# Optimization experiments

Hardware: AMD Instinct MI355X
Metric: run time of the kernel (lower is better)

Reference implementation:

```python
import jax, jax.numpy as jnp
import numpy as np

RAD_ORDER = 15
ANG_ORDER = 7
RAD_CUTOFF = 6.0
ANG_CUTOFF = 4.0
MIN_CUTOFF = 0.55
N_SPECIES = 2
N_ATOMS = 10000
MAX_NB = 32


def _typespin(n_species):
    # matches Fortran: even n skips zero -> {-1, 1} for 2 species
    vals = []
    s = int(-n_species / 2)
    for _ in range(n_species):
        if s == 0 and n_species % 2 == 0:
            s += 1
        vals.append(float(s))
        s += 1
    return jnp.asarray(vals, dtype=jnp.float32)


def _cheby_stack(x, order):
    # T_0..T_order of x, stacked on last axis
    Ts = [jnp.ones_like(x), x]
    for _ in range(2, order + 1):
        Ts.append(2.0 * x * Ts[-1] - Ts[-2])
    return jnp.stack(Ts[: order + 1], axis=-1)


def setup_inputs() -> dict:
    key = jax.random.key(0)
    k1, k2, k3 = jax.random.split(key, 3)
    positions = jax.random.normal(k1, (N_ATOMS, 3), dtype=jnp.float32) * 5.0
    species_indices = jax.random.randint(k2, (N_ATOMS,), 0, N_SPECIES)
    neighbor_indices = jax.random.randint(k3, (N_ATOMS, MAX_NB), 0, N_ATOMS)
    neighbor_vectors = jax.random.normal(jax.random.fold_in(key, 7), (N_ATOMS, MAX_NB, 3), dtype=jnp.float32) * 2.5
    return {
        "positions": positions,
        "species_indices": species_indices,
        "neighbor_indices": neighbor_indices,
        "neighbor_vectors": neighbor_vectors,
    }


def _features(positions, species_indices, neighbor_indices, neighbor_vectors):
    typespin = _typespin(N_SPECIES)
    ts_nb = typespin[species_indices[neighbor_indices]]  # [N, M]

    d = jnp.linalg.norm(neighbor_vectors, axis=-1)  # [N, M]
    d_safe = jnp.maximum(d, 1e-8)

    # ---------- radial ----------
    mask_r = ((d <= RAD_CUTOFF) & (d > MIN_CUTOFF)).astype(d.dtype)  # [N, M]
    x_r = jnp.clip(2.0 * (d - MIN_CUTOFF) / (RAD_CUTOFF - MIN_CUTOFF) - 1.0, -1.0, 1.0)
    fc_r = 0.5 * (jnp.cos(jnp.pi * jnp.minimum(d, RAD_CUTOFF) / RAD_CUTOFF) + 1.0)
    G_rad = _cheby_stack(x_r, RAD_ORDER) * (fc_r * mask_r)[..., None]  # [N, M, n_rad]
    rad_unw = G_rad.sum(axis=1)                          # [N, n_rad]
    rad_w = (G_rad * ts_nb[..., None]).sum(axis=1)       # [N, n_rad]

    # ---------- angular ----------
    mask_a = ((d <= ANG_CUTOFF) & (d > MIN_CUTOFF)).astype(d.dtype)  # [N, M]
    fc_a = 0.5 * (jnp.cos(jnp.pi * jnp.minimum(d, ANG_CUTOFF) / ANG_CUTOFF) + 1.0) * mask_a
    unit = neighbor_vectors / d_safe[..., None]          # [N, M, 3]
    cos = jnp.clip(jnp.einsum("nmd,nkd->nmk", unit, unit), -1.0, 1.0)  # [N, M, M]
    triu = jnp.triu(jnp.ones((MAX_NB, MAX_NB), dtype=d.dtype), k=1)
    w = fc_a[:, :, None] * fc_a[:, None, :] * triu       # [N, M, M] pair weight, j<k only
    w_ts = w * ts_nb[:, :, None] * ts_nb[:, None, :]

    # Chebyshev recurrence over cos(theta); accumulate per order to avoid [N,M,M,n_ang]
    ang_unw, ang_w = [], []
    T_prev = jnp.ones_like(cos)
    T_cur = cos
    for n in range(ANG_ORDER + 1):
        T_n = T_prev if n == 0 else (T_cur if n == 1 else 2.0 * cos * T_cur - T_prev)
        if n >= 2:
            T_prev, T_cur = T_cur, T_n
        ang_unw.append(jnp.einsum("nmk,nmk->n", w, T_n))
        ang_w.append(jnp.einsum("nmk,nmk->n", w_ts, T_n))
    ang_unw = jnp.stack(ang_unw, axis=1)  # [N, n_ang]
    ang_w = jnp.stack(ang_w, axis=1)

    # feature layout: [rad_unweighted, rad_typespin, ang_unweighted, ang_typespin]
    return jnp.concatenate([rad_unw, rad_w, ang_unw, ang_w], axis=1)  # [N, 48]


def reference(positions, species_indices, neighbor_indices, neighbor_vectors):
    return _features(positions, species_indices, neighbor_indices, neighbor_vectors)
```

## Files before the change

kernel.cpp:

```cpp
#include <hip/hip_runtime.h>

#define NATOMS 10000
#define MAXNB  32
#define NRAD   16
#define NANG   8
#define WPB    4
#define RSTRIDE 33

__global__ __launch_bounds__(256, 4) void cheby_desc_kernel(
    const int*   __restrict__ species,
    const int*   __restrict__ nb_idx,
    const float* __restrict__ nb_vec,
    float*       __restrict__ out)
{
    const int lane = threadIdx.x & 63;
    const int wv   = threadIdx.x >> 6;
    const int atom = blockIdx.x * WPB + wv;
    const int nb   = lane & 31;

    __shared__ float nbd[WPB][MAXNB][5];
    __shared__ float red[WPB][64][RSTRIDE];

    const float vx = nb_vec[(atom * MAXNB + nb) * 3 + 0];
    const float vy = nb_vec[(atom * MAXNB + nb) * 3 + 1];
    const float vz = nb_vec[(atom * MAXNB + nb) * 3 + 2];
    const int   ni = nb_idx[atom * MAXNB + nb];
    const float ts = (float)(2 * species[ni] - 1);

    const float d     = __builtin_amdgcn_sqrtf(vx * vx + vy * vy + vz * vz);
    const float inv_d = __builtin_amdgcn_rcpf(fmaxf(d, 1e-8f));
    const float ux = vx * inv_d, uy = vy * inv_d, uz = vz * inv_d;

    const float PI = 3.14159265358979323846f;

    float xr = 2.0f * (d - 0.55f) * (1.0f / (6.0f - 0.55f)) - 1.0f;
    xr = fminf(fmaxf(xr, -1.0f), 1.0f);
    const float fcr = 0.5f * (__cosf(fminf(d, 6.0f) * (PI / 6.0f)) + 1.0f);
    float g = ((d <= 6.0f) && (d > 0.55f)) ? fcr : 0.0f;
    if (lane >= 32) g *= ts;

    float rad[NRAD];
    {
        rad[0] = g;
        rad[1] = g * xr;
        float Tp = 1.0f, Tc = xr;
        const float x2 = xr + xr;
        #pragma unroll
        for (int n = 2; n < NRAD; ++n) {
            const float Tn = x2 * Tc - Tp;
            rad[n] = g * Tn;
            Tp = Tc; Tc = Tn;
        }
    }

    const float fca = ((d <= 4.0f) && (d > 0.55f))
                    ? 0.5f * (__cosf(fminf(d, 4.0f) * (PI / 4.0f)) + 1.0f) : 0.0f;
    const float fcats = fca * ts;

    if (lane < 32) {
        nbd[wv][nb][0] = ux;  nbd[wv][nb][1] = uy;  nbd[wv][nb][2] = uz;
        nbd[wv][nb][3] = fca; nbd[wv][nb][4] = fcats;
    }
    __syncthreads();

    float aU[NANG], aW[NANG];
    #pragma unroll
    for (int n = 0; n < NANG; ++n) { aU[n] = 0.0f; aW[n] = 0.0f; }

    const int half = lane >> 5;
    #pragma unroll
    for (int it = 0; it < 8; ++it) {
        const int o = 2 * it + 1 + half;
        const int k = (nb + o) & 31;
        const float kx   = nbd[wv][k][0];
        const float ky   = nbd[wv][k][1];
        const float kz   = nbd[wv][k][2];
        const float fk   = nbd[wv][k][3];
        const float fkts = nbd[wv][k][4];
        float c = ux * kx + uy * ky + uz * kz;
        c = fminf(fmaxf(c, -1.0f), 1.0f);
        float w   = fca   * fk;
        float wts = fcats * fkts;
        if (o == 16) { w *= 0.5f; wts *= 0.5f; }
        const float c2 = c + c;
        float Ta = 1.0f, Tb = c;
        aU[0] += w;     aW[0] += wts;
        aU[1] += w * c; aW[1] += wts * c;
        #pragma unroll
        for (int n = 2; n < NANG; ++n) {
            const float Tn = c2 * Tb - Ta;
            aU[n] += w * Tn;  aW[n] += wts * Tn;
            Ta = Tb; Tb = Tn;
        }
    }

    {
        float* rrow = &red[wv][lane][0];
        #pragma unroll
        for (int n = 0; n < NRAD; ++n) rrow[n] = rad[n];
        #pragma unroll
        for (int n = 0; n < NANG; ++n) { rrow[16 + n] = aU[n]; rrow[24 + n] = aW[n]; }
    }
    __syncthreads();

    const int   base = ((lane >> 4) & 1) * 32;
    const int   col  = (lane < 32) ? (lane & 15) : (16 + (lane & 15));
    const float* rcol = &red[wv][base][col];
    float s0 = 0.0f, s1 = 0.0f, s2 = 0.0f, s3 = 0.0f;
    #pragma unroll
    for (int i = 0; i < 32; i += 4) {
        s0 += rcol[(i + 0) * RSTRIDE];
        s1 += rcol[(i + 1) * RSTRIDE];
        s2 += rcol[(i + 2) * RSTRIDE];
        s3 += rcol[(i + 3) * RSTRIDE];
    }
    float v = (s0 + s1) + (s2 + s3);
    const float vp = __shfl_xor(v, 16, 64);
    if (lane >= 32) v += vp;
    if (lane < 48) out[atom * 48 + lane] = v;
}

extern "C" void kernel_launch(void* const* d_in, const int* in_sizes, int n_in,
                              void* d_out, int out_size, void* d_ws, size_t ws_size,
                              hipStream_t stream) {
    const int*   species = (const int*)  d_in[1];
    const int*   nbidx   = (const int*)  d_in[2];
    const float* nbvec   = (const float*)d_in[3];
    float*       out     = (float*)      d_out;

    const int blocks = NATOMS / WPB;
    cheby_desc_kernel<<<blocks, 256, 0, stream>>>(species, nbidx, nbvec, out);
}
```

Measured before the change: 13.61 us.

## Map two atoms per wavefront and replace block barriers with wave-level LDS fences

Each 64-lane wavefront now handles two atoms (one per 32-lane half) instead of duplicating the neighbors of one atom across both halves. Each half does the full 16-offset angular loop, so per-lane work doubles while the grid is halved. Neighbor data is packed into float4 in LDS, reduction rows are written as float4, and __syncthreads is replaced by an s_waitcnt lgkmcnt(0) fence because each wave only touches its own LDS slice. This relies on in-wave LDS ordering being enough without a barrier. Launch bounds drop to 2 and LDS per block grows, which lowers occupancy.

```diff
diff --git a/kernel.cpp b/kernel.cpp
--- a/kernel.cpp
+++ b/kernel.cpp
@@ -5,9 +5,11 @@
 #define NRAD   16
 #define NANG   8
 #define WPB    4
-#define RSTRIDE 33
+#define RSTRIDE 52
 
-__global__ __launch_bounds__(256, 4) void cheby_desc_kernel(
+#define WAVE_LDS_FENCE() asm volatile("s_waitcnt lgkmcnt(0)" ::: "memory")
+
+__global__ __launch_bounds__(256, 2) void cheby_desc_kernel(
     const int*   __restrict__ species,
     const int*   __restrict__ nb_idx,
     const float* __restrict__ nb_vec,
@@ -15,11 +17,14 @@
 {
     const int lane = threadIdx.x & 63;
     const int wv   = threadIdx.x >> 6;
-    const int atom = blockIdx.x * WPB + wv;
+    const int sub  = lane >> 5;
     const int nb   = lane & 31;
+    const int abase = blockIdx.x * (WPB * 2) + wv * 2;
+    const int atom  = abase + sub;
 
-    __shared__ float nbd[WPB][MAXNB][5];
-    __shared__ float red[WPB][64][RSTRIDE];
+    __shared__ float4 nbd4[WPB][64];
+    __shared__ float  nbdS[WPB][64];
+    __shared__ float  red[WPB][64][RSTRIDE];
 
     const float vx = nb_vec[(atom * MAXNB + nb) * 3 + 0];
     const float vy = nb_vec[(atom * MAXNB + nb) * 3 + 1];
@@ -36,8 +41,7 @@
     float xr = 2.0f * (d - 0.55f) * (1.0f / (6.0f - 0.55f)) - 1.0f;
     xr = fminf(fmaxf(xr, -1.0f), 1.0f);
     const float fcr = 0.5f * (__cosf(fminf(d, 6.0f) * (PI / 6.0f)) + 1.0f);
-    float g = ((d <= 6.0f) && (d > 0.55f)) ? fcr : 0.0f;
-    if (lane >= 32) g *= ts;
+    const float g = ((d <= 6.0f) && (d > 0.55f)) ? fcr : 0.0f;
 
     float rad[NRAD];
     {
@@ -57,29 +61,23 @@
                     ? 0.5f * (__cosf(fminf(d, 4.0f) * (PI / 4.0f)) + 1.0f) : 0.0f;
     const float fcats = fca * ts;
 
-    if (lane < 32) {
-        nbd[wv][nb][0] = ux;  nbd[wv][nb][1] = uy;  nbd[wv][nb][2] = uz;
-        nbd[wv][nb][3] = fca; nbd[wv][nb][4] = fcats;
-    }
-    __syncthreads();
+    nbd4[wv][lane] = make_float4(ux, uy, uz, fca);
+    nbdS[wv][lane] = fcats;
+    WAVE_LDS_FENCE();
 
     float aU[NANG], aW[NANG];
     #pragma unroll
     for (int n = 0; n < NANG; ++n) { aU[n] = 0.0f; aW[n] = 0.0f; }
 
-    const int half = lane >> 5;
+    const int kb = sub * 32;
     #pragma unroll
-    for (int it = 0; it < 8; ++it) {
-        const int o = 2 * it + 1 + half;
-        const int k = (nb + o) & 31;
-        const float kx   = nbd[wv][k][0];
-        const float ky   = nbd[wv][k][1];
-        const float kz   = nbd[wv][k][2];
-        const float fk   = nbd[wv][k][3];
-        const float fkts = nbd[wv][k][4];
-        float c = ux * kx + uy * ky + uz * kz;
+    for (int o = 1; o <= 16; ++o) {
+        const int k = kb + ((nb + o) & 31);
+        const float4 K   = nbd4[wv][k];
+        const float fkts = nbdS[wv][k];
+        float c = ux * K.x + uy * K.y + uz * K.z;
         c = fminf(fmaxf(c, -1.0f), 1.0f);
-        float w   = fca   * fk;
+        float w   = fca   * K.w;
         float wts = fcats * fkts;
         if (o == 16) { w *= 0.5f; wts *= 0.5f; }
         const float c2 = c + c;
@@ -95,29 +93,47 @@
     }
 
     {
-        float* rrow = &red[wv][lane][0];
+        float* rr = &red[wv][lane][0];
         #pragma unroll
-        for (int n = 0; n < NRAD; ++n) rrow[n] = rad[n];
+        for (int n = 0; n < NRAD; n += 4)
+            *(float4*)(rr + n) = make_float4(rad[n], rad[n+1], rad[n+2], rad[n+3]);
         #pragma unroll
-        for (int n = 0; n < NANG; ++n) { rrow[16 + n] = aU[n]; rrow[24 + n] = aW[n]; }
+        for (int n = 0; n < NRAD; n += 4)
+            *(float4*)(rr + 16 + n) = make_float4(ts*rad[n], ts*rad[n+1], ts*rad[n+2], ts*rad[n+3]);
+        *(float4*)(rr + 32) = make_float4(aU[0], aU[1], aU[2], aU[3]);
+        *(float4*)(rr + 36) = make_float4(aU[4], aU[5], aU[6], aU[7]);
+        *(float4*)(rr + 40) = make_float4(aW[0], aW[1], aW[2], aW[3]);
+        *(float4*)(rr + 44) = make_float4(aW[4], aW[5], aW[6], aW[7]);
     }
-    __syncthreads();
+    WAVE_LDS_FENCE();
 
-    const int   base = ((lane >> 4) & 1) * 32;
-    const int   col  = (lane < 32) ? (lane & 15) : (16 + (lane & 15));
-    const float* rcol = &red[wv][base][col];
-    float s0 = 0.0f, s1 = 0.0f, s2 = 0.0f, s3 = 0.0f;
-    #pragma unroll
-    for (int i = 0; i < 32; i += 4) {
-        s0 += rcol[(i + 0) * RSTRIDE];
-        s1 += rcol[(i + 1) * RSTRIDE];
-        s2 += rcol[(i + 2) * RSTRIDE];
-        s3 += rcol[(i + 3) * RSTRIDE];
+    {
+        const int s = (lane >= 48) ? 1 : 0;
+        const int c = lane - 48 * s;
+        const float* col = &red[wv][32 * s][c];
+        float s0 = 0.f, s1 = 0.f, s2 = 0.f, s3 = 0.f;
+        #pragma unroll
+        for (int i = 0; i < 32; i += 4) {
+            s0 += col[(i + 0) * RSTRIDE];
+            s1 += col[(i + 1) * RSTRIDE];
+            s2 += col[(i + 2) * RSTRIDE];
+            s3 += col[(i + 3) * RSTRIDE];
+        }
+        out[(abase + s) * 48 + c] = (s0 + s1) + (s2 + s3);
     }
-    float v = (s0 + s1) + (s2 + s3);
-    const float vp = __shfl_xor(v, 16, 64);
-    if (lane >= 32) v += vp;
-    if (lane < 48) out[atom * 48 + lane] = v;
+    if (lane < 32) {
+        const int c = 16 + lane;
+        const float* col = &red[wv][32][c];
+        float s0 = 0.f, s1 = 0.f, s2 = 0.f, s3 = 0.f;
+        #pragma unroll
+        for (int i = 0; i < 32; i += 4) {
+            s0 += col[(i + 0) * RSTRIDE];
+            s1 += col[(i + 1) * RSTRIDE];
+            s2 += col[(i + 2) * RSTRIDE];
+            s3 += col[(i + 3) * RSTRIDE];
+        }
+        out[(abase + 1) * 48 + c] = (s0 + s1) + (s2 + s3);
+    }
 }
 
 extern "C" void kernel_launch(void* const* d_in, const int* in_sizes, int n_in,
@@ -128,6 +144,6 @@
     const float* nbvec   = (const float*)d_in[3];
     float*       out     = (float*)      d_out;
 
-    const int blocks = NATOMS / WPB;
+    const int blocks = NATOMS / (WPB * 2);
     cheby_desc_kernel<<<blocks, 256, 0, stream>>>(species, nbidx, nbvec, out);
 }
```

Result: slower. 14.36 us (+5.5%).
